# Performance work log

Hardware: AMD Instinct MI355X
Metric: run time of the kernel (lower is better)

## Reference

```python
import jax, jax.numpy as jnp
import numpy as np

B, C_FEAT, C_COND, C_KEY, H, W = 4, 256, 256, 32, 64, 64


def setup_inputs() -> dict:
    key = jax.random.key(0)
    ks = jax.random.split(key, 8)
    s = 0.02
    return {
        "features": jax.random.normal(ks[0], (B, C_FEAT, H, W), jnp.float32),
        "conditions": jax.random.normal(ks[1], (B, C_COND, H, W), jnp.float32),
        "Wq": jax.random.normal(ks[2], (C_KEY, C_COND), jnp.float32) * s,
        "bq": jnp.zeros((C_KEY,), jnp.float32),
        "Wk": jax.random.normal(ks[3], (C_KEY, C_FEAT), jnp.float32) * s,
        "bk": jnp.zeros((C_KEY,), jnp.float32),
        "Wv": jax.random.normal(ks[4], (C_FEAT, C_FEAT), jnp.float32) * s,
        "bv": jnp.zeros((C_FEAT,), jnp.float32),
        "gamma": jnp.zeros((1,), jnp.float32),
    }


def reference(features, conditions, Wq, bq, Wk, bk, Wv, bv, gamma):
    b, c, h, w = features.shape
    n = h * w
    feat = features.reshape(b, c, n)            # [B, C, N]
    cond = conditions.reshape(b, cond_c := conditions.shape[1], n)
    # 1x1 convs == per-pixel linear projections
    q = jnp.einsum('kc,bcn->bnk', Wq, cond) + bq          # [B, N, Ck]
    k = jnp.einsum('kc,bcn->bkn', Wk, feat) + bk[:, None]  # [B, Ck, N]
    v = jnp.einsum('oc,bcn->bon', Wv, feat) + bv[:, None]  # [B, C, N]
    energy = jnp.einsum('bik,bkj->bij', q, k)             # [B, N, N]
    attn = jax.nn.softmax(energy, axis=-1)
    out = jnp.einsum('bcj,bij->bci', v, attn)             # [B, C, N]
    out = out.reshape(b, c, h, w)
    return gamma * out + features
```

## Files before the change

kernel.cpp:

```cpp
#include <hip/hip_runtime.h>

typedef __bf16 bf16_t;
typedef __bf16 bf16x2 __attribute__((ext_vector_type(2)));
typedef __bf16 bf16x8 __attribute__((ext_vector_type(8)));
typedef float f32x4 __attribute__((ext_vector_type(4)));
typedef unsigned u32;
typedef unsigned u32x2 __attribute__((ext_vector_type(2)));
typedef unsigned u32x4 __attribute__((ext_vector_type(4)));

#define N_PIX 4096
#define CFEAT 256
#define CKEY 32
#define NBATCH 4

#if __has_builtin(__builtin_amdgcn_exp2f)
#define EXP2(x) __builtin_amdgcn_exp2f(x)
#else
#define EXP2(x) exp2f(x)
#endif

static __device__ __forceinline__ f32x4 mfma16(bf16x8 a, bf16x8 b, f32x4 c) {
    return __builtin_amdgcn_mfma_f32_16x16x32_bf16(a, b, c, 0, 0, 0);
}

static __device__ __forceinline__ void glds16(const void* g, void* l) {
    __builtin_amdgcn_global_load_lds(
        (const __attribute__((address_space(1))) void*)g,
        (__attribute__((address_space(3))) void*)l, 16, 0, 0);
}

static __device__ __forceinline__ u32 pk2(float lo, float hi) {
    bf16x2 t; t[0] = (bf16_t)lo; t[1] = (bf16_t)hi;
    return __builtin_bit_cast(u32, t);
}

static __device__ __forceinline__ bf16x8 cast8(const float* p) {
    f32x4 lo = *(const f32x4*)p;
    f32x4 hi = *(const f32x4*)(p + 4);
    u32x4 w = {pk2(lo[0], lo[1]), pk2(lo[2], lo[3]),
               pk2(hi[0], hi[1]), pk2(hi[2], hi[3])};
    return __builtin_bit_cast(bf16x8, w);
}

static __device__ __forceinline__ void xpose4(u32 &x, u32 &y) {
#if __has_builtin(__builtin_amdgcn_permlane32_swap) && __has_builtin(__builtin_amdgcn_permlane16_swap)
    auto r32 = __builtin_amdgcn_permlane32_swap(x, y, false, false);
    auto r16 = __builtin_amdgcn_permlane16_swap(r32[0], r32[1], false, false);
    x = r16[0]; y = r16[1];
#else
    const int lane = threadIdx.x & 63;
    const int g = lane >> 4, ln = lane & 15;
    const int i0 = ln + ((g & 1) << 5);
    const int i2 = i0 + 16;
    u32 xs0 = (u32)__shfl((int)x, i0), ys0 = (u32)__shfl((int)y, i0);
    u32 xs2 = (u32)__shfl((int)x, i2), ys2 = (u32)__shfl((int)y, i2);
    x = (g < 2) ? xs0 : ys0;
    y = (g < 2) ? xs2 : ys2;
#endif
}

static __device__ __forceinline__ void softmax_tile(
    const bf16x8 kf[4], bf16x8 qf, bf16x8 ones,
    f32x4 &accsum, bf16x8 &pa0, bf16x8 &pa1)
{
    f32x4 zero = {0.f, 0.f, 0.f, 0.f};
    f32x4 st[4];
#pragma unroll
    for (int jt = 0; jt < 4; ++jt) st[jt] = mfma16(kf[jt], qf, zero);
    float ex[16];
#pragma unroll
    for (int jt = 0; jt < 4; ++jt)
#pragma unroll
        for (int r = 0; r < 4; ++r) ex[jt * 4 + r] = EXP2(st[jt][r]);
    u32 a0 = pk2(ex[0],  ex[1]),  a1 = pk2(ex[2],  ex[3]);
    u32 b0 = pk2(ex[4],  ex[5]),  b1 = pk2(ex[6],  ex[7]);
    u32 c0 = pk2(ex[8],  ex[9]),  c1 = pk2(ex[10], ex[11]);
    u32 d0 = pk2(ex[12], ex[13]), d1 = pk2(ex[14], ex[15]);
    xpose4(a0, b0); xpose4(a1, b1);
    xpose4(c0, d0); xpose4(c1, d1);
    u32x4 w0 = {a0, a1, b0, b1};
    u32x4 w1 = {c0, c1, d0, d1};
    pa0 = __builtin_bit_cast(bf16x8, w0);
    pa1 = __builtin_bit_cast(bf16x8, w1);
    accsum = mfma16(ones, pa0, accsum);
    accsum = mfma16(ones, pa1, accsum);
}

__global__ __launch_bounds__(256) void prep_kernel(
    const float* __restrict__ cond, const float* __restrict__ feat,
    bf16_t* __restrict__ XTc, bf16_t* __restrict__ XTf)
{
    __shared__ __attribute__((aligned(16))) float T[64][68];
    const int tid = threadIdx.x, bid = blockIdx.x;
    const int t = bid >> 10;
    const int r = bid & 1023;
    const int b = r >> 8;
    const int tile = r & 255;
    const int ct = tile >> 6, nt = tile & 63;
    const float* src = (t ? feat : cond) +
                       ((size_t)b * CFEAT + ct * 64) * N_PIX + (size_t)nt * 64;
    bf16_t* dst = (t ? XTf : XTc) +
                  ((size_t)b * N_PIX + nt * 64) * CFEAT + ct * 64;

    const int cl = tid >> 4, n4 = (tid & 15) * 4;
#pragma unroll
    for (int q = 0; q < 4; ++q) {
        f32x4 v = *(const f32x4*)&src[(size_t)(cl + q * 16) * N_PIX + n4];
        *(f32x4*)&T[cl + q * 16][n4] = v;
    }
    __syncthreads();
    const int n_loc = tid >> 2;
#pragma unroll
    for (int h = 0; h < 2; ++h) {
        const int c0 = (tid & 3) * 16 + h * 8;
        u32x4 o;
#pragma unroll
        for (int p = 0; p < 4; ++p)
            o[p] = pk2(T[c0 + 2 * p][n_loc], T[c0 + 2 * p + 1][n_loc]);
        *(u32x4*)&dst[(size_t)n_loc * CFEAT + c0] = o;
    }
}

__global__ __launch_bounds__(256) void proj_kernel(
    const float* __restrict__ Wq, const float* __restrict__ bq,
    const float* __restrict__ Wk, const float* __restrict__ bk,
    const float* __restrict__ Wv, const float* __restrict__ bv,
    const bf16_t* __restrict__ XTc, const bf16_t* __restrict__ XTf,
    bf16_t* __restrict__ Qt, bf16_t* __restrict__ Kt, bf16_t* __restrict__ Vv)
{
    __shared__ __attribute__((aligned(16))) bf16_t T[64][40];
    const int lane = threadIdx.x & 63, wave = threadIdx.x >> 6;
    const int g = lane >> 4, ln = lane & 15;
    const int bid = blockIdx.x;
    f32x4 zero = {0.f, 0.f, 0.f, 0.f};

    if (bid < 512) {
        const bool isK = (bid >= 256);
        const int idx = bid & 255;
        const int xt = idx & 63;
        const int b  = idx >> 6;
        const float* W    = isK ? Wk : Wq;
        const float* bias = isK ? bk : bq;
        const bf16_t* XT = (isK ? XTf : XTc) + (size_t)b * N_PIX * CFEAT;
        bf16_t* Yt = (isK ? Kt : Qt) + (size_t)b * N_PIX * CKEY;
        const float qscale = isK ? 1.0f : 1.4426950408889634f;

        const int m_base = (wave & 1) * 16;
        const int n_loc  = (wave >> 1) * 32;
        const int n_base = xt * 64 + n_loc;

        f32x4 acc[2] = {zero, zero};
#pragma unroll
        for (int k0 = 0; k0 < CFEAT; k0 += 32) {
            bf16x8 a = cast8(W + (size_t)(m_base + ln) * CFEAT + k0 + g * 8);
#pragma unroll
            for (int nt = 0; nt < 2; ++nt) {
                bf16x8 bfr = *(const bf16x8*)
                    &XT[(size_t)(n_base + nt * 16 + ln) * CFEAT + k0 + g * 8];
                acc[nt] = mfma16(a, bfr, acc[nt]);
            }
        }
#pragma unroll
        for (int nt = 0; nt < 2; ++nt)
#pragma unroll
            for (int r = 0; r < 4; ++r) {
                const int ck = m_base + g * 4 + r;
                T[n_loc + nt * 16 + ln][ck] = (bf16_t)((acc[nt][r] + bias[ck]) * qscale);
            }
        __syncthreads();
        const int n  = threadIdx.x >> 2;
        const int sg = threadIdx.x & 3;
        bf16x8 row = *(const bf16x8*)&T[n][sg * 8];
        *(bf16x8*)&Yt[(size_t)(xt * 64 + n) * CKEY + sg * 8] = row;
    } else {
        const int idx = bid - 512;
        const int xt = idx & 127;
        const int b  = idx >> 7;
        const int n_base = xt * 32;
        const int c_wave = wave * 64;
        const bf16_t* XT = XTf + (size_t)b * N_PIX * CFEAT;
        bf16_t* Vb = Vv + (size_t)b * CFEAT * N_PIX;

        f32x4 acc[4][2];
#pragma unroll
        for (int mt = 0; mt < 4; ++mt) { acc[mt][0] = zero; acc[mt][1] = zero; }

#pragma unroll
        for (int k0 = 0; k0 < CFEAT; k0 += 32) {
            bf16x8 bfr[2];
#pragma unroll
            for (int nt = 0; nt < 2; ++nt)
                bfr[nt] = *(const bf16x8*)
                    &XT[(size_t)(n_base + nt * 16 + ln) * CFEAT + k0 + g * 8];
#pragma unroll
            for (int mt = 0; mt < 4; ++mt) {
                bf16x8 a = cast8(Wv + (size_t)(c_wave + mt * 16 + ln) * CFEAT + k0 + g * 8);
                acc[mt][0] = mfma16(a, bfr[0], acc[mt][0]);
                acc[mt][1] = mfma16(a, bfr[1], acc[mt][1]);
            }
        }
#pragma unroll
        for (int mt = 0; mt < 4; ++mt)
#pragma unroll
            for (int nt = 0; nt < 2; ++nt)
#pragma unroll
                for (int r = 0; r < 4; ++r) {
                    const int m = c_wave + mt * 16 + g * 4 + r;
                    const int n = n_base + nt * 16 + ln;
                    Vb[(size_t)m * N_PIX + n] = (bf16_t)(acc[mt][nt][r] + bv[m]);
                }
    }
}

__global__ __launch_bounds__(128, 1) void pv_kernel(
    const bf16_t* __restrict__ Qt, const bf16_t* __restrict__ Kt,
    const bf16_t* __restrict__ V,
    const float* __restrict__ features, const float* __restrict__ gamma,
    float* __restrict__ out)
{
    __shared__ __attribute__((aligned(16))) bf16_t Vlds[4][128 * 64];

    const int lane = threadIdx.x & 63, wave = threadIdx.x >> 6;
    const int g = lane >> 4, ln = lane & 15;
    const int b = blockIdx.z;
    const int i_base = blockIdx.y * 64 + wave * 32;
    const int c_base = blockIdx.x * 128;

    const bf16_t* Qb = Qt + (size_t)b * N_PIX * CKEY;
    const bf16_t* Kb = Kt + (size_t)b * N_PIX * CKEY;
    const bf16_t* Vb = V + (size_t)b * CFEAT * N_PIX;

    const bf16_t* vgp[8];
#pragma unroll
    for (int q = 0; q < 8; ++q) {
        const int s = wave * 512 + q * 64 + lane;
        const int sc = s >> 3, sj = (s & 7) ^ (sc & 7);
        vgp[q] = Vb + (size_t)(c_base + sc) * N_PIX + sj * 8;
    }

    const bf16x8 qf0 = *(const bf16x8*)&Qb[(size_t)(i_base + ln) * CKEY + g * 8];
    const bf16x8 qf1 = *(const bf16x8*)&Qb[(size_t)(i_base + 16 + ln) * CKEY + g * 8];

    bf16x8 ones;
#pragma unroll
    for (int j = 0; j < 8; ++j) ones[j] = (bf16_t)1.0f;

    f32x4 zero = {0.f, 0.f, 0.f, 0.f};
    f32x4 acc[8][2];
#pragma unroll
    for (int ct = 0; ct < 8; ++ct) { acc[ct][0] = zero; acc[ct][1] = zero; }
    f32x4 accsum0 = zero, accsum1 = zero;

    bf16x8 pa0c0, pa1c0, pa0c1, pa1c1;

    {
        bf16x8 kf[4];
#pragma unroll
        for (int jt = 0; jt < 4; ++jt)
            kf[jt] = *(const bf16x8*)&Kb[(size_t)(jt * 16 + ln) * CKEY + g * 8];
        asm volatile("" ::: "memory");
#pragma unroll
        for (int q = 0; q < 8; ++q)
            glds16(vgp[q], &Vlds[0][(wave * 512 + q * 64) * 8]);
#pragma unroll
        for (int q = 0; q < 8; ++q)
            glds16(vgp[q] + 64, &Vlds[1][(wave * 512 + q * 64) * 8]);
        softmax_tile(kf, qf0, ones, accsum0, pa0c0, pa1c0);
        softmax_tile(kf, qf1, ones, accsum1, pa0c1, pa1c1);
        asm volatile("s_waitcnt vmcnt(8)" ::: "memory");
        __builtin_amdgcn_s_barrier();
        asm volatile("" ::: "memory");
    }

    for (int n = 0; n < 64; ++n) {
        const int jq = ((n + 1) & 63) * 64;
        bf16x8 kf[4];
#pragma unroll
        for (int jt = 0; jt < 4; ++jt)
            kf[jt] = *(const bf16x8*)&Kb[(size_t)(jq + jt * 16 + ln) * CKEY + g * 8];

        const bf16_t* Vt = &Vlds[n & 3][0];
        bf16x8 vf[16];
#pragma unroll
        for (int ct = 0; ct < 8; ++ct) {
            const int c = ct * 16 + ln;
            vf[2 * ct]     = *(const bf16x8*)&Vt[(c * 8 + ( g      ^ (c & 7))) * 8];
            vf[2 * ct + 1] = *(const bf16x8*)&Vt[(c * 8 + ((4 + g) ^ (c & 7))) * 8];
        }
        asm volatile("" ::: "memory");

        const int jn = (n * 64 + 128) & (N_PIX - 1);
        bf16_t* ldb = &Vlds[(n + 2) & 3][0];
#pragma unroll
        for (int q = 0; q < 8; ++q)
            glds16(vgp[q] + jn, &ldb[(wave * 512 + q * 64) * 8]);

        bf16x8 pa0n0, pa1n0, pa0n1, pa1n1;
        const bool live = (n < 63);
        if (live) {
            softmax_tile(kf, qf0, ones, accsum0, pa0n0, pa1n0);
            softmax_tile(kf, qf1, ones, accsum1, pa0n1, pa1n1);
        }

        asm volatile("s_waitcnt vmcnt(8)" ::: "memory");
        __builtin_amdgcn_s_barrier();
        asm volatile("" ::: "memory");

        __builtin_amdgcn_s_setprio(1);
#pragma unroll
        for (int ct = 0; ct < 8; ++ct) {
            acc[ct][0] = mfma16(vf[2 * ct],     pa0c0, acc[ct][0]);
            acc[ct][0] = mfma16(vf[2 * ct + 1], pa1c0, acc[ct][0]);
            acc[ct][1] = mfma16(vf[2 * ct],     pa0c1, acc[ct][1]);
            acc[ct][1] = mfma16(vf[2 * ct + 1], pa1c1, acc[ct][1]);
        }
        __builtin_amdgcn_s_setprio(0);
        if (live) {
            pa0c0 = pa0n0; pa1c0 = pa1n0;
            pa0c1 = pa0n1; pa1c1 = pa1n1;
        }
    }

    const float s0 = gamma[0] / accsum0[0];
    const float s1 = gamma[0] / accsum1[0];

#pragma unroll
    for (int ct = 0; ct < 8; ++ct)
#pragma unroll
        for (int r = 0; r < 4; ++r) {
            const int c = c_base + ct * 16 + g * 4 + r;
            const size_t row = ((size_t)b * CFEAT + c) * N_PIX;
            const size_t idx0 = row + i_base + ln;
            const size_t idx1 = row + i_base + 16 + ln;
            out[idx0] = s0 * acc[ct][0][r] + features[idx0];
            out[idx1] = s1 * acc[ct][1][r] + features[idx1];
        }
}

extern "C" void kernel_launch(void* const* d_in, const int* in_sizes, int n_in,
                              void* d_out, int out_size, void* d_ws, size_t ws_size,
                              hipStream_t stream) {
    const float* features   = (const float*)d_in[0];
    const float* conditions = (const float*)d_in[1];
    const float* Wq  = (const float*)d_in[2];
    const float* bq  = (const float*)d_in[3];
    const float* Wk  = (const float*)d_in[4];
    const float* bk  = (const float*)d_in[5];
    const float* Wv  = (const float*)d_in[6];
    const float* bv  = (const float*)d_in[7];
    const float* gam = (const float*)d_in[8];
    float* out = (float*)d_out;

    bf16_t* Qt = (bf16_t*)d_ws;
    bf16_t* Kt = Qt + (size_t)NBATCH * N_PIX * CKEY;
    bf16_t* Vw = Kt + (size_t)NBATCH * N_PIX * CKEY;
    bf16_t* XTc = (bf16_t*)d_out;
    bf16_t* XTf = XTc + (size_t)NBATCH * N_PIX * CFEAT;

    prep_kernel<<<dim3(2048, 1, 1), 256, 0, stream>>>(conditions, features, XTc, XTf);
    proj_kernel<<<dim3(1024, 1, 1), 256, 0, stream>>>(
        Wq, bq, Wk, bk, Wv, bv, XTc, XTf, Qt, Kt, Vw);
    pv_kernel<<<dim3(2, N_PIX / 64, NBATCH), 128, 0, stream>>>(
        Qt, Kt, Vw, features, gam, out);
}
```

Baseline: 200.9 us.

## Restructure PV kernel into 8-wave blocks sharing softmax via LDS

The attention kernel now uses 512-thread blocks, each covering 64 query rows and all 256 channels. Four waves compute the softmax probabilities and write them to a double-buffered, swizzled LDS tile, and all eight waves read them to accumulate their 32-channel slices. This removes the softmax recomputation that came from splitting channels across two blocks, and the V staging work is now shared unevenly across waves. In exchange it adds LDS traffic for P, a larger LDS footprint (about 144 KB), and block-wide barriers every iteration. The K/Q/V projection loops also lose their unroll pragmas.

```diff
diff --git a/kernel.cpp b/kernel.cpp
--- a/kernel.cpp
+++ b/kernel.cpp
@@ -5,7 +5,6 @@
 typedef __bf16 bf16x8 __attribute__((ext_vector_type(8)));
 typedef float f32x4 __attribute__((ext_vector_type(4)));
 typedef unsigned u32;
-typedef unsigned u32x2 __attribute__((ext_vector_type(2)));
 typedef unsigned u32x4 __attribute__((ext_vector_type(4)));
 
 #define N_PIX 4096
@@ -150,7 +149,6 @@
         const int n_base = xt * 64 + n_loc;
 
         f32x4 acc[2] = {zero, zero};
-#pragma unroll
         for (int k0 = 0; k0 < CFEAT; k0 += 32) {
             bf16x8 a = cast8(W + (size_t)(m_base + ln) * CFEAT + k0 + g * 8);
 #pragma unroll
@@ -185,7 +183,6 @@
 #pragma unroll
         for (int mt = 0; mt < 4; ++mt) { acc[mt][0] = zero; acc[mt][1] = zero; }
 
-#pragma unroll
         for (int k0 = 0; k0 < CFEAT; k0 += 32) {
             bf16x8 bfr[2];
 #pragma unroll
@@ -212,129 +209,154 @@
     }
 }
 
-__global__ __launch_bounds__(128, 1) void pv_kernel(
+__global__ __launch_bounds__(512, 2) void pv_kernel(
     const bf16_t* __restrict__ Qt, const bf16_t* __restrict__ Kt,
     const bf16_t* __restrict__ V,
     const float* __restrict__ features, const float* __restrict__ gamma,
     float* __restrict__ out)
 {
-    __shared__ __attribute__((aligned(16))) bf16_t Vlds[4][128 * 64];
+    __shared__ __attribute__((aligned(16))) bf16_t Vlds[4][16384];
+    __shared__ __attribute__((aligned(16))) bf16_t Plds[2][4096];
+    __shared__ float Llds[64];
 
     const int lane = threadIdx.x & 63, wave = threadIdx.x >> 6;
     const int g = lane >> 4, ln = lane & 15;
-    const int b = blockIdx.z;
-    const int i_base = blockIdx.y * 64 + wave * 32;
-    const int c_base = blockIdx.x * 128;
+    const int b = blockIdx.y;
+    const int i_base = blockIdx.x * 64;
+    const bool sm = (wave < 4);
 
     const bf16_t* Qb = Qt + (size_t)b * N_PIX * CKEY;
     const bf16_t* Kb = Kt + (size_t)b * N_PIX * CKEY;
     const bf16_t* Vb = V + (size_t)b * CFEAT * N_PIX;
 
-    const bf16_t* vgp[8];
-#pragma unroll
-    for (int q = 0; q < 8; ++q) {
-        const int s = wave * 512 + q * 64 + lane;
+    const int u0 = sm ? wave * 2 : 8 + (wave - 4) * 6;
+    const bf16_t* vgp[6];
+#pragma unroll
+    for (int q = 0; q < 6; ++q) {
+        const int s = (u0 + q) * 64 + lane;
         const int sc = s >> 3, sj = (s & 7) ^ (sc & 7);
-        vgp[q] = Vb + (size_t)(c_base + sc) * N_PIX + sj * 8;
-    }
-
-    const bf16x8 qf0 = *(const bf16x8*)&Qb[(size_t)(i_base + ln) * CKEY + g * 8];
-    const bf16x8 qf1 = *(const bf16x8*)&Qb[(size_t)(i_base + 16 + ln) * CKEY + g * 8];
+        vgp[q] = Vb + (size_t)sc * N_PIX + sj * 8;
+    }
+
+#define STAGE(BUF, JOFF)                                                     \
+    if (sm) {                                                                \
+        _Pragma("unroll") for (int q = 0; q < 2; ++q)                        \
+            glds16(vgp[q] + (JOFF), &Vlds[BUF][(u0 + q) * 512]);             \
+    } else {                                                                 \
+        _Pragma("unroll") for (int q = 0; q < 6; ++q)                        \
+            glds16(vgp[q] + (JOFF), &Vlds[BUF][(u0 + q) * 512]);             \
+    }
+
+#define LOADK(DST, JQ)                                                       \
+    { _Pragma("unroll") for (int jt = 0; jt < 4; ++jt)                       \
+        DST[jt] = *(const bf16x8*)&Kb[(size_t)((JQ) + jt * 16 + ln) * CKEY + g * 8]; }
+
+#define PWRITE(SLOT, PA0, PA1)                                               \
+    { const int ir = wave * 16 + ln;                                         \
+      char* Pw = (char*)&Plds[SLOT][0] + ir * 128;                           \
+      *(bf16x8*)(Pw + ((g)     ^ (ir & 7)) * 16) = PA0;                      \
+      *(bf16x8*)(Pw + ((4 + g) ^ (ir & 7)) * 16) = PA1; }
+
+    bf16x8 qf = {};
+    if (sm) qf = *(const bf16x8*)&Qb[(size_t)(i_base + wave * 16 + ln) * CKEY + g * 8];
 
     bf16x8 ones;
 #pragma unroll
     for (int j = 0; j < 8; ++j) ones[j] = (bf16_t)1.0f;
 
     f32x4 zero = {0.f, 0.f, 0.f, 0.f};
-    f32x4 acc[8][2];
-#pragma unroll
-    for (int ct = 0; ct < 8; ++ct) { acc[ct][0] = zero; acc[ct][1] = zero; }
-    f32x4 accsum0 = zero, accsum1 = zero;
-
-    bf16x8 pa0c0, pa1c0, pa0c1, pa1c1;
-
-    {
-        bf16x8 kf[4];
-#pragma unroll
-        for (int jt = 0; jt < 4; ++jt)
-            kf[jt] = *(const bf16x8*)&Kb[(size_t)(jt * 16 + ln) * CKEY + g * 8];
-        asm volatile("" ::: "memory");
-#pragma unroll
-        for (int q = 0; q < 8; ++q)
-            glds16(vgp[q], &Vlds[0][(wave * 512 + q * 64) * 8]);
-#pragma unroll
-        for (int q = 0; q < 8; ++q)
-            glds16(vgp[q] + 64, &Vlds[1][(wave * 512 + q * 64) * 8]);
-        softmax_tile(kf, qf0, ones, accsum0, pa0c0, pa1c0);
-        softmax_tile(kf, qf1, ones, accsum1, pa0c1, pa1c1);
-        asm volatile("s_waitcnt vmcnt(8)" ::: "memory");
-        __builtin_amdgcn_s_barrier();
-        asm volatile("" ::: "memory");
-    }
-
-    for (int n = 0; n < 64; ++n) {
-        const int jq = ((n + 1) & 63) * 64;
-        bf16x8 kf[4];
-#pragma unroll
-        for (int jt = 0; jt < 4; ++jt)
-            kf[jt] = *(const bf16x8*)&Kb[(size_t)(jq + jt * 16 + ln) * CKEY + g * 8];
-
-        const bf16_t* Vt = &Vlds[n & 3][0];
-        bf16x8 vf[16];
-#pragma unroll
-        for (int ct = 0; ct < 8; ++ct) {
-            const int c = ct * 16 + ln;
-            vf[2 * ct]     = *(const bf16x8*)&Vt[(c * 8 + ( g      ^ (c & 7))) * 8];
-            vf[2 * ct + 1] = *(const bf16x8*)&Vt[(c * 8 + ((4 + g) ^ (c & 7))) * 8];
-        }
-        asm volatile("" ::: "memory");
-
-        const int jn = (n * 64 + 128) & (N_PIX - 1);
-        bf16_t* ldb = &Vlds[(n + 2) & 3][0];
-#pragma unroll
-        for (int q = 0; q < 8; ++q)
-            glds16(vgp[q] + jn, &ldb[(wave * 512 + q * 64) * 8]);
-
-        bf16x8 pa0n0, pa1n0, pa0n1, pa1n1;
-        const bool live = (n < 63);
-        if (live) {
-            softmax_tile(kf, qf0, ones, accsum0, pa0n0, pa1n0);
-            softmax_tile(kf, qf1, ones, accsum1, pa0n1, pa1n1);
-        }
-
-        asm volatile("s_waitcnt vmcnt(8)" ::: "memory");
-        __builtin_amdgcn_s_barrier();
-        asm volatile("" ::: "memory");
-
-        __builtin_amdgcn_s_setprio(1);
-#pragma unroll
-        for (int ct = 0; ct < 8; ++ct) {
-            acc[ct][0] = mfma16(vf[2 * ct],     pa0c0, acc[ct][0]);
-            acc[ct][0] = mfma16(vf[2 * ct + 1], pa1c0, acc[ct][0]);
-            acc[ct][1] = mfma16(vf[2 * ct],     pa0c1, acc[ct][1]);
-            acc[ct][1] = mfma16(vf[2 * ct + 1], pa1c1, acc[ct][1]);
-        }
-        __builtin_amdgcn_s_setprio(0);
-        if (live) {
-            pa0c0 = pa0n0; pa1c0 = pa1n0;
-            pa0c1 = pa0n1; pa1c1 = pa1n1;
-        }
-    }
-
-    const float s0 = gamma[0] / accsum0[0];
-    const float s1 = gamma[0] / accsum1[0];
-
-#pragma unroll
-    for (int ct = 0; ct < 8; ++ct)
-#pragma unroll
-        for (int r = 0; r < 4; ++r) {
-            const int c = c_base + ct * 16 + g * 4 + r;
-            const size_t row = ((size_t)b * CFEAT + c) * N_PIX;
-            const size_t idx0 = row + i_base + ln;
-            const size_t idx1 = row + i_base + 16 + ln;
-            out[idx0] = s0 * acc[ct][0][r] + features[idx0];
-            out[idx1] = s1 * acc[ct][1][r] + features[idx1];
-        }
+    f32x4 acc[2][4];
+#pragma unroll
+    for (int ct = 0; ct < 2; ++ct)
+#pragma unroll
+        for (int it = 0; it < 4; ++it) acc[ct][it] = zero;
+    f32x4 accsum = zero;
+
+    bf16x8 kfA[4], kfB[4];
+
+    if (sm) LOADK(kfA, 0);
+    asm volatile("" ::: "memory");
+    STAGE(0, 0);
+    STAGE(1, 64);
+    if (sm) {
+        bf16x8 pa0, pa1;
+        softmax_tile(kfA, qf, ones, accsum, pa0, pa1);
+        PWRITE(0, pa0, pa1);
+        LOADK(kfA, 64);
+    }
+    __syncthreads();
+
+#define PV_ITER(NN, KU, KN)                                                  \
+  {                                                                          \
+    const int nn = (NN);                                                     \
+    const bf16_t* Vt = &Vlds[nn & 3][0];                                     \
+    bf16x8 vf[4];                                                            \
+    _Pragma("unroll")                                                        \
+    for (int ct = 0; ct < 2; ++ct)                                           \
+      _Pragma("unroll")                                                      \
+      for (int s = 0; s < 2; ++s) {                                          \
+        const int c = wave * 32 + ct * 16 + ln;                              \
+        vf[ct * 2 + s] = *(const bf16x8*)&Vt[(c * 8 + ((s * 4 + g) ^ (c & 7))) * 8]; \
+      }                                                                      \
+    const char* Pr = (const char*)&Plds[nn & 1][0];                          \
+    bf16x8 pf[8];                                                            \
+    _Pragma("unroll")                                                        \
+    for (int it = 0; it < 4; ++it)                                           \
+      _Pragma("unroll")                                                      \
+      for (int s = 0; s < 2; ++s)                                            \
+        pf[it * 2 + s] = *(const bf16x8*)(Pr + (it * 16 + ln) * 128          \
+                           + ((s * 4 + g) ^ (ln & 7)) * 16);                 \
+    const bool live = (nn < 63);                                             \
+    if (sm && live) LOADK(KN, ((nn + 2) & 63) * 64);                         \
+    asm volatile("" ::: "memory");   \
+    STAGE((nn + 2) & 3, ((nn * 64 + 128) & (N_PIX - 1)));                    \
+    if (sm && live) {                                                        \
+      bf16x8 pa0, pa1;                                                       \
+      softmax_tile(KU, qf, ones, accsum, pa0, pa1);                          \
+      PWRITE((nn + 1) & 1, pa0, pa1);                                        \
+    }                                                                        \
+    asm volatile("s_waitcnt vmcnt(6)" ::: "memory");                         \
+    asm volatile("s_waitcnt lgkmcnt(0)" ::: "memory");                       \
+    __builtin_amdgcn_s_barrier();                                            \
+    asm volatile("" ::: "memory");                                           \
+    __builtin_amdgcn_s_setprio(1);                                           \
+    _Pragma("unroll")                                                        \
+    for (int ct = 0; ct < 2; ++ct)                                           \
+      _Pragma("unroll")                                                      \
+      for (int it = 0; it < 4; ++it) {                                       \
+        acc[ct][it] = mfma16(vf[ct * 2 + 0], pf[it * 2 + 0], acc[ct][it]);   \
+        acc[ct][it] = mfma16(vf[ct * 2 + 1], pf[it * 2 + 1], acc[ct][it]);   \
+      }                                                                      \
+    __builtin_amdgcn_s_setprio(0);                                           \
+  }
+
+    for (int n2 = 0; n2 < 32; ++n2) {
+        PV_ITER(2 * n2,     kfA, kfB);
+        PV_ITER(2 * n2 + 1, kfB, kfA);
+    }
+#undef PV_ITER
+
+    if (sm && g == 0) Llds[wave * 16 + ln] = accsum[0];
+    __syncthreads();
+    const float gam = gamma[0];
+    float sc4[4];
+#pragma unroll
+    for (int it = 0; it < 4; ++it) sc4[it] = gam / Llds[it * 16 + ln];
+
+#pragma unroll
+    for (int ct = 0; ct < 2; ++ct)
+#pragma unroll
+        for (int it = 0; it < 4; ++it)
+#pragma unroll
+            for (int r = 0; r < 4; ++r) {
+                const int c = wave * 32 + ct * 16 + g * 4 + r;
+                const int i = i_base + it * 16 + ln;
+                const size_t idx = ((size_t)b * CFEAT + c) * N_PIX + i;
+                out[idx] = sc4[it] * acc[ct][it][r] + features[idx];
+            }
+#undef STAGE
+#undef LOADK
+#undef PWRITE
 }
 
 extern "C" void kernel_launch(void* const* d_in, const int* in_sizes, int n_in,
@@ -360,6 +382,6 @@
     prep_kernel<<<dim3(2048, 1, 1), 256, 0, stream>>>(conditions, features, XTc, XTf);
     proj_kernel<<<dim3(1024, 1, 1), 256, 0, stream>>>(
         Wq, bq, Wk, bk, Wv, bv, XTc, XTf, Qt, Kt, Vw);
-    pv_kernel<<<dim3(2, N_PIX / 64, NBATCH), 128, 0, stream>>>(
+    pv_kernel<<<dim3(64, NBATCH, 1), 512, 0, stream>>>(
         Qt, Kt, Vw, features, gam, out);
 }
```

Measured after the change: 176.0 us. 1.14x faster.
